# Optimization experiments

Measured on AMD Instinct MI355X. Metric: run time of the kernel, lower is better.

The kernel has to match this reference:

```python
import jax, jax.numpy as jnp
import numpy as np

B, S, E, H = 2, 2048, 1024, 16
DK = E // H


def setup_inputs() -> dict:
    key = jax.random.key(0)
    ks = jax.random.split(key, 10)
    x = jax.random.normal(ks[0], (B, S, E), dtype=jnp.float32)
    mask = jax.random.randint(ks[1], (B, S, S), 0, 2).astype(bool)
    scale = 1.0 / np.sqrt(E)
    def lin(k):
        kw, kb = jax.random.split(k)
        W = jax.random.uniform(kw, (E, E), minval=-scale, maxval=scale, dtype=jnp.float32)
        b = jax.random.uniform(kb, (E,), minval=-scale, maxval=scale, dtype=jnp.float32)
        return W, b
    Wq, bq = lin(ks[2])
    Wk, bk = lin(ks[3])
    Wv, bv = lin(ks[4])
    Wo, bo = lin(ks[5])
    return {"x": x, "mask": mask, "Wq": Wq, "bq": bq, "Wk": Wk, "bk": bk,
            "Wv": Wv, "bv": bv, "Wo": Wo, "bo": bo}


def reference(x, mask, Wq, bq, Wk, bk, Wv, bv, Wo, bo):
    # projections (torch Linear: y = x @ W.T + b)
    q = x @ Wq.T + bq
    k = x @ Wk.T + bk
    v = x @ Wv.T + bv
    # separate heads: [B,S,E] -> [B,H,S,DK]
    def split(t):
        return t.reshape(B, S, H, DK).transpose(0, 2, 1, 3)
    q, k, v = split(q), split(k), split(v)
    scores = jnp.einsum("bhqd,bhkd->bhqk", q, k) / jnp.sqrt(jnp.float32(DK))
    # masked_fill: positions where mask is True get -1e9 (mask broadcast over heads)
    scores = jnp.where(mask[:, None, :, :], jnp.float32(-1e9), scores)
    attn = jax.nn.softmax(scores, axis=-1)  # dropout is identity in eval
    out = jnp.einsum("bhqk,bhkd->bhqd", attn, v)
    out = out.transpose(0, 2, 1, 3).reshape(B, S, E)  # combine heads
    return out @ Wo.T + bo
```

## Files before the change

kernel.cpp:

```cpp
#include <hip/hip_runtime.h>
#include <hip/hip_bf16.h>


typedef __attribute__((ext_vector_type(8))) short short8;
typedef __attribute__((ext_vector_type(4))) float f32x4;
typedef __attribute__((ext_vector_type(16))) float f32x16;

#define MFMA16(a, b, c) __builtin_amdgcn_mfma_f32_16x16x32_bf16(a, b, c, 0, 0, 0)
#define MFMA32(a, b, c) __builtin_amdgcn_mfma_f32_32x32x16_bf16(a, b, c, 0, 0, 0)

#define BATCH 2
#define SEQ   2048
#define EMB   1024
#define HEADS 16
#define DKK   64

typedef __hip_bfloat16 bf16;

static __device__ __forceinline__ short bf16b(float f) {
    union { bf16 h; short s; } u;
    u.h = __float2bfloat16(f);
    return u.s;
}
static __device__ __forceinline__ unsigned cvtpk(float lo, float hi) {
    unsigned r;
    asm("v_cvt_pk_bf16_f32 %0, %1, %2" : "=v"(r) : "v"(lo), "v"(hi));
    return r;
}
static __device__ __forceinline__ void swap32(unsigned &a, unsigned &b) {
    asm("v_permlane32_swap_b32 %0, %1" : "+v"(a), "+v"(b));
}
static __device__ __forceinline__ short8 ld8k(const bf16* p) {
    return *(const short8*)p;
}
static __device__ __forceinline__ short8 ld8kf(const float* p) {
    const f32x4 a = *(const f32x4*)p;
    const f32x4 b = *(const f32x4*)(p + 4);
    short8 r;
    r[0] = bf16b(a[0]); r[1] = bf16b(a[1]); r[2] = bf16b(a[2]); r[3] = bf16b(a[3]);
    r[4] = bf16b(b[0]); r[5] = bf16b(b[1]); r[6] = bf16b(b[2]); r[7] = bf16b(b[3]);
    return r;
}

static __device__ __forceinline__ void glds16(const bf16* g, bf16* l) {
    __builtin_amdgcn_global_load_lds(
        (const __attribute__((address_space(1))) void*)g,
        (__attribute__((address_space(3))) void*)l, 16, 0, 0);
}

__global__ void detect_kernel(const unsigned int* __restrict__ mw,
                              int* __restrict__ flags) {
    __shared__ int mbyte;
    if (threadIdx.x == 0) mbyte = 0;
    __syncthreads();
    int mb = 0;
    for (int i = threadIdx.x; i < 4096; i += 256)
        if (mw[i] > 1u) mb = 1;
    if (mb) atomicOr(&mbyte, 1);
    __syncthreads();
    if (threadIdx.x == 0) { flags[0] = 1; flags[1] = mbyte; }
}

__global__ __launch_bounds__(256) void pack_mask(
        const void* __restrict__ mp, unsigned* __restrict__ Mp,
        const int* __restrict__ flags) {
    const bool m8 = flags[1] != 0;
    const int T = blockIdx.x * 256 + threadIdx.x;
    const int lane = T & 63, g = T >> 6;
    const int wvv = g & 3;
    const int qb  = (g >> 2) & 15;
    const int it  = (g >> 6) & 31;
    const int b   = g >> 11;
    const int l32 = lane & 31, hi = lane >> 5;
    const int q = qb * 128 + wvv * 32 + l32;
    const size_t rowb = ((size_t)(b * 2048 + q)) * 2048;

    unsigned out[8];
    if (m8) {
        const unsigned char* p8 = (const unsigned char*)mp;
#pragma unroll
        for (int k = 0; k < 8; ++k) {
            const int kb = k >> 2, tt = (k >> 1) & 1, u = k & 1;
            const int key0 = it * 64 + kb * 32 + tt * 16 + hi * 8 + u * 4;
            const unsigned v = *(const unsigned*)(p8 + rowb + key0);
            unsigned w = 0;
#pragma unroll
            for (int r = 0; r < 4; ++r)
                w |= ((((v >> (8 * r)) & 0xFFu) == 0u) ? 0xFFu : 0u) << (8 * r);
            out[k] = w;
        }
    } else {
        const int* p32 = (const int*)mp;
#pragma unroll
        for (int k = 0; k < 8; ++k) {
            const int kb = k >> 2, tt = (k >> 1) & 1, u = k & 1;
            const int key0 = it * 64 + kb * 32 + tt * 16 + hi * 8 + u * 4;
            const int4 v = *(const int4*)(p32 + rowb + key0);
            unsigned w = 0;
            w |=  (v.x == 0) ? 0xFFu : 0u;
            w |= ((v.y == 0) ? 0xFFu : 0u) << 8;
            w |= ((v.z == 0) ? 0xFFu : 0u) << 16;
            w |= ((v.w == 0) ? 0xFFu : 0u) << 24;
            out[k] = w;
        }
    }
    unsigned* dst = Mp + (size_t)g * 512 + lane * 8;
    *(uint4*)dst       = make_uint4(out[0], out[1], out[2], out[3]);
    *(uint4*)(dst + 4) = make_uint4(out[4], out[5], out[6], out[7]);
}

__global__ __launch_bounds__(256) void cvt_all(
        const float* __restrict__ x,  const float* __restrict__ wq,
        const float* __restrict__ wk, const float* __restrict__ wv,
        const float* __restrict__ wo,
        bf16* __restrict__ xb,  bf16* __restrict__ wqb,
        bf16* __restrict__ wkb, bf16* __restrict__ wvb,
        bf16* __restrict__ wob) {
    const int bid = blockIdx.x;
    const float* s; bf16* d; int base;
    if (bid < 2048)      { s = x;  d = xb;  base = bid; }
    else if (bid < 2560) { s = wq; d = wqb; base = bid - 2048; }
    else if (bid < 3072) { s = wk; d = wkb; base = bid - 2560; }
    else if (bid < 3584) { s = wv; d = wvb; base = bid - 3072; }
    else                 { s = wo; d = wob; base = bid - 3584; }
    const int i = (base * 256 + threadIdx.x) * 8;
    *(short8*)(d + i) = ld8kf(s + i);
}

__global__ __launch_bounds__(256) void gemm_qkv_staged(
        const bf16* __restrict__ X,
        const bf16* __restrict__ Wq, const bf16* __restrict__ Wk,
        const bf16* __restrict__ Wv,
        const float* __restrict__ bq, const float* __restrict__ bk,
        const float* __restrict__ bv,
        bf16* __restrict__ qo, bf16* __restrict__ ko, bf16* __restrict__ vo) {
    __shared__ bf16 As[2][128 * 32];
    __shared__ bf16 Bs[2][128 * 32];

    const int t = threadIdx.x, lane = t & 63;
    const int wv = t >> 6;
    const int mb = blockIdx.x / 24, nb = blockIdx.x % 24;
    const int m0 = mb * 128;
    const int n0g = nb * 128;
    const int sel = n0g >> 10;
    const int n0 = n0g & 1023;
    const bf16* W     = sel == 0 ? Wq : (sel == 1 ? Wk : Wv);
    const float* bias = sel == 0 ? bq : (sel == 1 ? bk : bv);
    bf16* out         = sel == 0 ? qo : (sel == 1 ? ko : vo);
    const float oscale = sel == 0 ? 0.18033688011f : 1.0f;

    const int wr = wv >> 1, wc = wv & 1;
    const int m_off = wr * 64, n_off = wc * 64;
    const int l16 = lane & 15, quad = lane >> 4;

    int srow[2], sg[2];
#pragma unroll
    for (int i = 0; i < 2; ++i) {
        const int c = i * 256 + t;
        srow[i] = c >> 2;
        sg[i]   = (c & 3) ^ (srow[i] & 3);
    }

    f32x4 acc[4][4];
#pragma unroll
    for (int i = 0; i < 4; ++i)
#pragma unroll
        for (int j = 0; j < 4; ++j)
            acc[i][j] = (f32x4){0.f, 0.f, 0.f, 0.f};

#pragma unroll
    for (int i = 0; i < 2; ++i) {
        glds16(X + (m0 + srow[i]) * 1024 + sg[i] * 8, &As[0][(i * 256 + t) * 8]);
        glds16(W + (n0 + srow[i]) * 1024 + sg[i] * 8, &Bs[0][(i * 256 + t) * 8]);
    }

    for (int it = 0; it < 32; ++it) {
        __syncthreads();
        if (it < 31) {
            const int ktn = (it + 1) * 32;
            const int nb_ = (it + 1) & 1;
#pragma unroll
            for (int i = 0; i < 2; ++i) {
                glds16(X + (m0 + srow[i]) * 1024 + ktn + sg[i] * 8,
                       &As[nb_][(i * 256 + t) * 8]);
                glds16(W + (n0 + srow[i]) * 1024 + ktn + sg[i] * 8,
                       &Bs[nb_][(i * 256 + t) * 8]);
            }
        }
        const bf16* Ab = As[it & 1];
        const bf16* Bb = Bs[it & 1];
        short8 af[4], bfr[4];
#pragma unroll
        for (int ii = 0; ii < 4; ++ii) {
            const int row = m_off + ii * 16 + l16;
            const int slot = quad ^ (row & 3);
            af[ii] = *(const short8*)(Ab + row * 32 + slot * 8);
        }
#pragma unroll
        for (int jj = 0; jj < 4; ++jj) {
            const int row = n_off + jj * 16 + l16;
            const int slot = quad ^ (row & 3);
            bfr[jj] = *(const short8*)(Bb + row * 32 + slot * 8);
        }
#pragma unroll
        for (int ii = 0; ii < 4; ++ii)
#pragma unroll
            for (int jj = 0; jj < 4; ++jj)
                acc[ii][jj] = MFMA16(af[ii], bfr[jj], acc[ii][jj]);
    }

#pragma unroll
    for (int j = 0; j < 4; ++j) {
        const int nl = n0 + n_off + j * 16 + l16;
        const float bj = bias[nl];
        const int h = nl >> 6, d = nl & 63;
#pragma unroll
        for (int i = 0; i < 4; ++i) {
#pragma unroll
            for (int r = 0; r < 4; ++r) {
                const int m = m0 + m_off + i * 16 + quad * 4 + r;
                const float v = (acc[i][j][r] + bj) * oscale;
                const int bb = m >> 11, ss = m & 2047;
                const int idx = (sel == 2)
                    ? ((bb * HEADS + h) * DKK + d) * SEQ + ss
                    : ((bb * HEADS + h) * SEQ + ss) * DKK + d;
                out[idx] = __float2bfloat16(v);
            }
        }
    }
}

__global__ __launch_bounds__(256) void gemm_out_staged(
        const bf16* __restrict__ X,
        const bf16* __restrict__ W, const float* __restrict__ bias,
        float* __restrict__ out) {
    __shared__ bf16 As[2][128 * 32];
    __shared__ bf16 Bs[2][64 * 32];

    const int t = threadIdx.x, lane = t & 63;
    const int wv = t >> 6;
    const int mb = blockIdx.x >> 4, nb = blockIdx.x & 15;
    const int m0 = mb * 128, n0 = nb * 64;
    const int wr = wv >> 1, wc = wv & 1;
    const int m_off = wr * 64, n_off = wc * 32;
    const int l16 = lane & 15, quad = lane >> 4;

    int srow[2], sg[2];
#pragma unroll
    for (int i = 0; i < 2; ++i) {
        const int c = i * 256 + t;
        srow[i] = c >> 2;
        sg[i]   = (c & 3) ^ (srow[i] & 3);
    }
    const int brow = t >> 2;
    const int bslot = (t & 3) ^ (brow & 3);

    f32x4 acc[4][2];
#pragma unroll
    for (int i = 0; i < 4; ++i)
#pragma unroll
        for (int j = 0; j < 2; ++j)
            acc[i][j] = (f32x4){0.f, 0.f, 0.f, 0.f};

#pragma unroll
    for (int i = 0; i < 2; ++i)
        glds16(X + (m0 + srow[i]) * 1024 + sg[i] * 8, &As[0][(i * 256 + t) * 8]);
    glds16(W + (n0 + brow) * 1024 + bslot * 8, &Bs[0][t * 8]);

    for (int it = 0; it < 32; ++it) {
        __syncthreads();
        if (it < 31) {
            const int ktn = (it + 1) * 32;
            const int nb_ = (it + 1) & 1;
#pragma unroll
            for (int i = 0; i < 2; ++i)
                glds16(X + (m0 + srow[i]) * 1024 + ktn + sg[i] * 8,
                       &As[nb_][(i * 256 + t) * 8]);
            glds16(W + (n0 + brow) * 1024 + ktn + bslot * 8, &Bs[nb_][t * 8]);
        }
        const bf16* Ab = As[it & 1];
        const bf16* Bb = Bs[it & 1];
        short8 af[4], bfr[2];
#pragma unroll
        for (int ii = 0; ii < 4; ++ii) {
            const int row = m_off + ii * 16 + l16;
            const int slot = quad ^ (row & 3);
            af[ii] = *(const short8*)(Ab + row * 32 + slot * 8);
        }
#pragma unroll
        for (int jj = 0; jj < 2; ++jj) {
            const int row = n_off + jj * 16 + l16;
            const int slot = quad ^ (row & 3);
            bfr[jj] = *(const short8*)(Bb + row * 32 + slot * 8);
        }
#pragma unroll
        for (int ii = 0; ii < 4; ++ii)
#pragma unroll
            for (int jj = 0; jj < 2; ++jj)
                acc[ii][jj] = MFMA16(af[ii], bfr[jj], acc[ii][jj]);
    }

#pragma unroll
    for (int j = 0; j < 2; ++j) {
        const int n = n0 + n_off + j * 16 + l16;
        const float bj = bias[n];
#pragma unroll
        for (int i = 0; i < 4; ++i) {
#pragma unroll
            for (int r = 0; r < 4; ++r) {
                const int m = m0 + m_off + i * 16 + quad * 4 + r;
                out[m * 1024 + n] = acc[i][j][r] + bj;
            }
        }
    }
}

__global__ __launch_bounds__(256, 2) void attn_kernel(
        const bf16* __restrict__ Qw,
        const bf16* __restrict__ Kw,
        const bf16* __restrict__ Vw,
        const unsigned* __restrict__ Mp,
        bf16* __restrict__ attn_out) {
    const int t = threadIdx.x;
    const int lane = t & 63;
    const int wv   = t >> 6;
    const int l32 = lane & 31, hi = lane >> 5;
    const int h = blockIdx.y, b = blockIdx.z;
    const int bh = b * HEADS + h;
    const int qb = blockIdx.x;
    const int qb0 = qb * 128;

    const bf16* Q  = Qw + bh * SEQ * DKK;
    const bf16* Kp = Kw + bh * SEQ * DKK;
    const bf16* Vt = Vw + bh * DKK * SEQ;

    __shared__ bf16 Ks[2][4096];
    __shared__ bf16 Vs[2][4096];

    short8 qf[4];
#pragma unroll
    for (int ks = 0; ks < 4; ++ks)
        qf[ks] = ld8k(Q + (qb0 + wv * 32 + l32) * DKK + ks * 16 + hi * 8);

    const short ob = bf16b(1.0f);
    short8 ones;
#pragma unroll
    for (int e = 0; e < 8; ++e) ones[e] = ob;

    f32x16 oA = {}, oB = {}, lacc = {};
    const f32x16 z16 = {};

    int srow[2], sg[2];
#pragma unroll
    for (int i = 0; i < 2; ++i) {
        const int c = i * 256 + t;
        srow[i] = c >> 3;
        sg[i]   = (c & 7) ^ (srow[i] & 7);
    }
#pragma unroll
    for (int i = 0; i < 2; ++i)
        glds16(Kp + srow[i] * DKK + sg[i] * 8, &Ks[0][(i * 256 + t) * 8]);
#pragma unroll
    for (int i = 0; i < 2; ++i)
        glds16(Vt + srow[i] * SEQ + sg[i] * 8, &Vs[0][(i * 256 + t) * 8]);

    const unsigned* mp_it =
        Mp + ((size_t)((b * 32) * 16 + qb) * 4 + wv) * 512 + lane * 8;

    for (int it = 0; it < 32; ++it) {
        __syncthreads();
        if (it < 31) {
            const int nb_ = (it + 1) & 1;
            const int ktn = (it + 1) * 64;
#pragma unroll
            for (int i = 0; i < 2; ++i)
                glds16(Kp + (ktn + srow[i]) * DKK + sg[i] * 8,
                       &Ks[nb_][(i * 256 + t) * 8]);
#pragma unroll
            for (int i = 0; i < 2; ++i)
                glds16(Vt + srow[i] * SEQ + ktn + sg[i] * 8,
                       &Vs[nb_][(i * 256 + t) * 8]);
        }
        const uint4 mA = *(const uint4*)mp_it;
        const uint4 mB = *(const uint4*)(mp_it + 4);
        mp_it += 32768;

        const bf16* Kb = Ks[it & 1];
        const bf16* Vb = Vs[it & 1];

        short8 kf0[4], kf1[4];
#pragma unroll
        for (int ks = 0; ks < 4; ++ks) {
            const int sl = (((ks * 2 + hi) ^ (l32 & 7))) * 8;
            kf0[ks] = *(const short8*)(Kb + l32 * 64 + sl);
            kf1[ks] = *(const short8*)(Kb + (32 + l32) * 64 + sl);
        }

        f32x16 s0, s1;
        __builtin_amdgcn_s_setprio(1);
        s0 = MFMA32(kf0[0], qf[0], z16);
        s0 = MFMA32(kf0[1], qf[1], s0);
        s0 = MFMA32(kf0[2], qf[2], s0);
        s0 = MFMA32(kf0[3], qf[3], s0);
        s1 = MFMA32(kf1[0], qf[0], z16);
        s1 = MFMA32(kf1[1], qf[1], s1);
        s1 = MFMA32(kf1[2], qf[2], s1);
        s1 = MFMA32(kf1[3], qf[3], s1);
        __builtin_amdgcn_s_setprio(0);

        {
            unsigned c0 = cvtpk(__builtin_exp2f(s0[0]),  __builtin_exp2f(s0[1]));
            unsigned c1 = cvtpk(__builtin_exp2f(s0[2]),  __builtin_exp2f(s0[3]));
            unsigned c2 = cvtpk(__builtin_exp2f(s0[4]),  __builtin_exp2f(s0[5]));
            unsigned c3 = cvtpk(__builtin_exp2f(s0[6]),  __builtin_exp2f(s0[7]));
            unsigned c4 = cvtpk(__builtin_exp2f(s0[8]),  __builtin_exp2f(s0[9]));
            unsigned c5 = cvtpk(__builtin_exp2f(s0[10]), __builtin_exp2f(s0[11]));
            unsigned c6 = cvtpk(__builtin_exp2f(s0[12]), __builtin_exp2f(s0[13]));
            unsigned c7 = cvtpk(__builtin_exp2f(s0[14]), __builtin_exp2f(s0[15]));
            swap32(c0, c2); swap32(c1, c3); swap32(c4, c6); swap32(c5, c7);
            union { short8 v; unsigned w[4]; } p0, p1;
            p0.w[0] = c0 & __builtin_amdgcn_perm(0u, mA.x, 0x01010000u);
            p0.w[1] = c1 & __builtin_amdgcn_perm(0u, mA.x, 0x03030202u);
            p0.w[2] = c2 & __builtin_amdgcn_perm(0u, mA.y, 0x01010000u);
            p0.w[3] = c3 & __builtin_amdgcn_perm(0u, mA.y, 0x03030202u);
            p1.w[0] = c4 & __builtin_amdgcn_perm(0u, mA.z, 0x01010000u);
            p1.w[1] = c5 & __builtin_amdgcn_perm(0u, mA.z, 0x03030202u);
            p1.w[2] = c6 & __builtin_amdgcn_perm(0u, mA.w, 0x01010000u);
            p1.w[3] = c7 & __builtin_amdgcn_perm(0u, mA.w, 0x03030202u);

            const int sl0 = ((0 + hi) ^ (l32 & 7)) * 8;
            const int sl1 = ((2 + hi) ^ (l32 & 7)) * 8;
            const short8 vf00 = *(const short8*)(Vb + l32 * 64 + sl0);
            const short8 vf10 = *(const short8*)(Vb + (32 + l32) * 64 + sl0);
            const short8 vf01 = *(const short8*)(Vb + l32 * 64 + sl1);
            const short8 vf11 = *(const short8*)(Vb + (32 + l32) * 64 + sl1);
            __builtin_amdgcn_s_setprio(1);
            lacc = MFMA32(p0.v, ones, lacc);
            oA = MFMA32(p0.v, vf00, oA);
            oB = MFMA32(p0.v, vf10, oB);
            lacc = MFMA32(p1.v, ones, lacc);
            oA = MFMA32(p1.v, vf01, oA);
            oB = MFMA32(p1.v, vf11, oB);
            __builtin_amdgcn_s_setprio(0);
        }
        {
            unsigned c0 = cvtpk(__builtin_exp2f(s1[0]),  __builtin_exp2f(s1[1]));
            unsigned c1 = cvtpk(__builtin_exp2f(s1[2]),  __builtin_exp2f(s1[3]));
            unsigned c2 = cvtpk(__builtin_exp2f(s1[4]),  __builtin_exp2f(s1[5]));
            unsigned c3 = cvtpk(__builtin_exp2f(s1[6]),  __builtin_exp2f(s1[7]));
            unsigned c4 = cvtpk(__builtin_exp2f(s1[8]),  __builtin_exp2f(s1[9]));
            unsigned c5 = cvtpk(__builtin_exp2f(s1[10]), __builtin_exp2f(s1[11]));
            unsigned c6 = cvtpk(__builtin_exp2f(s1[12]), __builtin_exp2f(s1[13]));
            unsigned c7 = cvtpk(__builtin_exp2f(s1[14]), __builtin_exp2f(s1[15]));
            swap32(c0, c2); swap32(c1, c3); swap32(c4, c6); swap32(c5, c7);
            union { short8 v; unsigned w[4]; } p0, p1;
            p0.w[0] = c0 & __builtin_amdgcn_perm(0u, mB.x, 0x01010000u);
            p0.w[1] = c1 & __builtin_amdgcn_perm(0u, mB.x, 0x03030202u);
            p0.w[2] = c2 & __builtin_amdgcn_perm(0u, mB.y, 0x01010000u);
            p0.w[3] = c3 & __builtin_amdgcn_perm(0u, mB.y, 0x03030202u);
            p1.w[0] = c4 & __builtin_amdgcn_perm(0u, mB.z, 0x01010000u);
            p1.w[1] = c5 & __builtin_amdgcn_perm(0u, mB.z, 0x03030202u);
            p1.w[2] = c6 & __builtin_amdgcn_perm(0u, mB.w, 0x01010000u);
            p1.w[3] = c7 & __builtin_amdgcn_perm(0u, mB.w, 0x03030202u);

            const int sl0 = ((4 + hi) ^ (l32 & 7)) * 8;
            const int sl1 = ((6 + hi) ^ (l32 & 7)) * 8;
            const short8 vf00 = *(const short8*)(Vb + l32 * 64 + sl0);
            const short8 vf10 = *(const short8*)(Vb + (32 + l32) * 64 + sl0);
            const short8 vf01 = *(const short8*)(Vb + l32 * 64 + sl1);
            const short8 vf11 = *(const short8*)(Vb + (32 + l32) * 64 + sl1);
            __builtin_amdgcn_s_setprio(1);
            lacc = MFMA32(p0.v, ones, lacc);
            oA = MFMA32(p0.v, vf00, oA);
            oB = MFMA32(p0.v, vf10, oB);
            lacc = MFMA32(p1.v, ones, lacc);
            oA = MFMA32(p1.v, vf01, oA);
            oB = MFMA32(p1.v, vf11, oB);
            __builtin_amdgcn_s_setprio(0);
        }
    }

#pragma unroll
    for (int r = 0; r < 16; ++r) {
        const int qrow = (r & 3) + 8 * (r >> 2) + 4 * hi;
        const float inv = 1.0f / lacc[r];
        const int q = qb0 + wv * 32 + qrow;
        bf16* orow = attn_out + (b * SEQ + q) * EMB + h * DKK;
        orow[l32]      = __float2bfloat16(oA[r] * inv);
        orow[32 + l32] = __float2bfloat16(oB[r] * inv);
    }
}

extern "C" void kernel_launch(void* const* d_in, const int* in_sizes, int n_in,
                              void* d_out, int out_size, void* d_ws, size_t ws_size,
                              hipStream_t stream) {
    char* ws = (char*)d_ws;
    const size_t MB = 1024 * 1024;
    int*      flags = (int*)ws;
    bf16*     wob   = (bf16*)(ws + 256);
    bf16*     wqb   = (bf16*)(ws + 256 + 2 * MB);
    bf16*     wkb   = (bf16*)(ws + 256 + 4 * MB);
    bf16*     wvb   = (bf16*)(ws + 256 + 6 * MB);
    unsigned* Mp    = (unsigned*)(ws + 256 + 2 * MB);
    bf16*     xb    = (bf16*)(ws + 256 + 10 * MB);
    bf16*     k_ws  = (bf16*)(ws + 256 + 18 * MB);
    bf16*     attn_ws = xb;

    bf16* q_ws = (bf16*)d_out;
    bf16* v_ws = (bf16*)d_out + 4194304;

    detect_kernel<<<1, 256, 0, stream>>>((const unsigned int*)d_in[1], flags);

    cvt_all<<<4096, 256, 0, stream>>>(
        (const float*)d_in[0], (const float*)d_in[2], (const float*)d_in[4],
        (const float*)d_in[6], (const float*)d_in[8],
        xb, wqb, wkb, wvb, wob);

    gemm_qkv_staged<<<768, 256, 0, stream>>>(
        xb, wqb, wkb, wvb,
        (const float*)d_in[3], (const float*)d_in[5], (const float*)d_in[7],
        q_ws, k_ws, v_ws);

    pack_mask<<<1024, 256, 0, stream>>>(d_in[1], Mp, flags);

    attn_kernel<<<dim3(SEQ / 128, HEADS, BATCH), 256, 0, stream>>>(
        q_ws, k_ws, v_ws, Mp, attn_ws);

    gemm_out_staged<<<512, 256, 0, stream>>>(
        attn_ws, wob, (const float*)d_in[9], (float*)d_out);
}
```

Before: 250.6 us.

## Triple-buffer K/V tiles with explicit vmcnt waits and remap block order

The attention kernel's K/V shared-memory staging grows from double to triple buffering. Tiles are prefetched two iterations ahead, and the full __syncthreads is replaced by an s_waitcnt vmcnt plus raw barrier so newer loads stay in flight. The packed-mask loads are also prefetched one iteration early. The grid becomes 1D with a swizzled block-to-(batch, head, qblock) mapping, likely to group blocks sharing K/V across XCDs for L2 reuse. The cost is 50% more LDS per block, which may hurt occupancy, and the hand-counted vmcnt must match the real number of outstanding loads.

```diff
diff --git a/kernel.cpp b/kernel.cpp
--- a/kernel.cpp
+++ b/kernel.cpp
@@ -325,17 +325,19 @@
     const int lane = t & 63;
     const int wv   = t >> 6;
     const int l32 = lane & 31, hi = lane >> 5;
-    const int h = blockIdx.y, b = blockIdx.z;
-    const int bh = b * HEADS + h;
-    const int qb = blockIdx.x;
+    const int bid = blockIdx.x;
+    const int w   = ((bid & 7) << 6) | (bid >> 3);
+    const int qb  = w & 15;
+    const int bh  = w >> 4;
+    const int b   = bh >> 4;
     const int qb0 = qb * 128;
 
     const bf16* Q  = Qw + bh * SEQ * DKK;
     const bf16* Kp = Kw + bh * SEQ * DKK;
     const bf16* Vt = Vw + bh * DKK * SEQ;
 
-    __shared__ bf16 Ks[2][4096];
-    __shared__ bf16 Vs[2][4096];
+    __shared__ bf16 Ks[3][4096];
+    __shared__ bf16 Vs[3][4096];
 
     short8 qf[4];
 #pragma unroll
@@ -357,36 +359,44 @@
         srow[i] = c >> 3;
         sg[i]   = (c & 7) ^ (srow[i] & 7);
     }
-#pragma unroll
-    for (int i = 0; i < 2; ++i)
-        glds16(Kp + srow[i] * DKK + sg[i] * 8, &Ks[0][(i * 256 + t) * 8]);
-#pragma unroll
-    for (int i = 0; i < 2; ++i)
-        glds16(Vt + srow[i] * SEQ + sg[i] * 8, &Vs[0][(i * 256 + t) * 8]);
+
+#define STAGE_TILE(ktn, bufi)                                                  \
+    do {                                                                       \
+        _Pragma("unroll")                                                      \
+        for (int i_ = 0; i_ < 2; ++i_)                                         \
+            glds16(Kp + ((ktn) + srow[i_]) * DKK + sg[i_] * 8,                 \
+                   &Ks[bufi][(i_ * 256 + t) * 8]);                             \
+        _Pragma("unroll")                                                      \
+        for (int i_ = 0; i_ < 2; ++i_)                                         \
+            glds16(Vt + srow[i_] * SEQ + (ktn) + sg[i_] * 8,                   \
+                   &Vs[bufi][(i_ * 256 + t) * 8]);                             \
+    } while (0)
 
     const unsigned* mp_it =
         Mp + ((size_t)((b * 32) * 16 + qb) * 4 + wv) * 512 + lane * 8;
 
+    STAGE_TILE(0, 0);
+    uint4 mcA = *(const uint4*)mp_it;
+    uint4 mcB = *(const uint4*)(mp_it + 4);
+    mp_it += 32768;
+    STAGE_TILE(64, 1);
+
     for (int it = 0; it < 32; ++it) {
-        __syncthreads();
+        if (it < 31) asm volatile("s_waitcnt vmcnt(6)" ::: "memory");
+        else         asm volatile("s_waitcnt vmcnt(0)" ::: "memory");
+        __builtin_amdgcn_s_barrier();
+        __builtin_amdgcn_sched_barrier(0);
+
+        uint4 mnA, mnB;
         if (it < 31) {
-            const int nb_ = (it + 1) & 1;
-            const int ktn = (it + 1) * 64;
-#pragma unroll
-            for (int i = 0; i < 2; ++i)
-                glds16(Kp + (ktn + srow[i]) * DKK + sg[i] * 8,
-                       &Ks[nb_][(i * 256 + t) * 8]);
-#pragma unroll
-            for (int i = 0; i < 2; ++i)
-                glds16(Vt + srow[i] * SEQ + ktn + sg[i] * 8,
-                       &Vs[nb_][(i * 256 + t) * 8]);
-        }
-        const uint4 mA = *(const uint4*)mp_it;
-        const uint4 mB = *(const uint4*)(mp_it + 4);
-        mp_it += 32768;
-
-        const bf16* Kb = Ks[it & 1];
-        const bf16* Vb = Vs[it & 1];
+            mnA = *(const uint4*)mp_it;
+            mnB = *(const uint4*)(mp_it + 4);
+            mp_it += 32768;
+        }
+        if (it < 30) STAGE_TILE((it + 2) * 64, (it + 2) % 3);
+
+        const bf16* Kb = Ks[it % 3];
+        const bf16* Vb = Vs[it % 3];
 
         short8 kf0[4], kf1[4];
 #pragma unroll
@@ -419,14 +429,14 @@
             unsigned c7 = cvtpk(__builtin_exp2f(s0[14]), __builtin_exp2f(s0[15]));
             swap32(c0, c2); swap32(c1, c3); swap32(c4, c6); swap32(c5, c7);
             union { short8 v; unsigned w[4]; } p0, p1;
-            p0.w[0] = c0 & __builtin_amdgcn_perm(0u, mA.x, 0x01010000u);
-            p0.w[1] = c1 & __builtin_amdgcn_perm(0u, mA.x, 0x03030202u);
-            p0.w[2] = c2 & __builtin_amdgcn_perm(0u, mA.y, 0x01010000u);
-            p0.w[3] = c3 & __builtin_amdgcn_perm(0u, mA.y, 0x03030202u);
-            p1.w[0] = c4 & __builtin_amdgcn_perm(0u, mA.z, 0x01010000u);
-            p1.w[1] = c5 & __builtin_amdgcn_perm(0u, mA.z, 0x03030202u);
-            p1.w[2] = c6 & __builtin_amdgcn_perm(0u, mA.w, 0x01010000u);
-            p1.w[3] = c7 & __builtin_amdgcn_perm(0u, mA.w, 0x03030202u);
+            p0.w[0] = c0 & __builtin_amdgcn_perm(0u, mcA.x, 0x01010000u);
+            p0.w[1] = c1 & __builtin_amdgcn_perm(0u, mcA.x, 0x03030202u);
+            p0.w[2] = c2 & __builtin_amdgcn_perm(0u, mcA.y, 0x01010000u);
+            p0.w[3] = c3 & __builtin_amdgcn_perm(0u, mcA.y, 0x03030202u);
+            p1.w[0] = c4 & __builtin_amdgcn_perm(0u, mcA.z, 0x01010000u);
+            p1.w[1] = c5 & __builtin_amdgcn_perm(0u, mcA.z, 0x03030202u);
+            p1.w[2] = c6 & __builtin_amdgcn_perm(0u, mcA.w, 0x01010000u);
+            p1.w[3] = c7 & __builtin_amdgcn_perm(0u, mcA.w, 0x03030202u);
 
             const int sl0 = ((0 + hi) ^ (l32 & 7)) * 8;
             const int sl1 = ((2 + hi) ^ (l32 & 7)) * 8;
@@ -454,14 +464,14 @@
             unsigned c7 = cvtpk(__builtin_exp2f(s1[14]), __builtin_exp2f(s1[15]));
             swap32(c0, c2); swap32(c1, c3); swap32(c4, c6); swap32(c5, c7);
             union { short8 v; unsigned w[4]; } p0, p1;
-            p0.w[0] = c0 & __builtin_amdgcn_perm(0u, mB.x, 0x01010000u);
-            p0.w[1] = c1 & __builtin_amdgcn_perm(0u, mB.x, 0x03030202u);
-            p0.w[2] = c2 & __builtin_amdgcn_perm(0u, mB.y, 0x01010000u);
-            p0.w[3] = c3 & __builtin_amdgcn_perm(0u, mB.y, 0x03030202u);
-            p1.w[0] = c4 & __builtin_amdgcn_perm(0u, mB.z, 0x01010000u);
-            p1.w[1] = c5 & __builtin_amdgcn_perm(0u, mB.z, 0x03030202u);
-            p1.w[2] = c6 & __builtin_amdgcn_perm(0u, mB.w, 0x01010000u);
-            p1.w[3] = c7 & __builtin_amdgcn_perm(0u, mB.w, 0x03030202u);
+            p0.w[0] = c0 & __builtin_amdgcn_perm(0u, mcB.x, 0x01010000u);
+            p0.w[1] = c1 & __builtin_amdgcn_perm(0u, mcB.x, 0x03030202u);
+            p0.w[2] = c2 & __builtin_amdgcn_perm(0u, mcB.y, 0x01010000u);
+            p0.w[3] = c3 & __builtin_amdgcn_perm(0u, mcB.y, 0x03030202u);
+            p1.w[0] = c4 & __builtin_amdgcn_perm(0u, mcB.z, 0x01010000u);
+            p1.w[1] = c5 & __builtin_amdgcn_perm(0u, mcB.z, 0x03030202u);
+            p1.w[2] = c6 & __builtin_amdgcn_perm(0u, mcB.w, 0x01010000u);
+            p1.w[3] = c7 & __builtin_amdgcn_perm(0u, mcB.w, 0x03030202u);
 
             const int sl0 = ((4 + hi) ^ (l32 & 7)) * 8;
             const int sl1 = ((6 + hi) ^ (l32 & 7)) * 8;
@@ -478,14 +488,16 @@
             oB = MFMA32(p1.v, vf11, oB);
             __builtin_amdgcn_s_setprio(0);
         }
-    }
+        if (it < 31) { mcA = mnA; mcB = mnB; }
+    }
+#undef STAGE_TILE
 
 #pragma unroll
     for (int r = 0; r < 16; ++r) {
         const int qrow = (r & 3) + 8 * (r >> 2) + 4 * hi;
         const float inv = 1.0f / lacc[r];
         const int q = qb0 + wv * 32 + qrow;
-        bf16* orow = attn_out + (b * SEQ + q) * EMB + h * DKK;
+        bf16* orow = attn_out + (b * SEQ + q) * EMB + (bh & 15) * DKK;
         orow[l32]      = __float2bfloat16(oA[r] * inv);
         orow[32 + l32] = __float2bfloat16(oB[r] * inv);
     }
@@ -523,8 +535,7 @@
 
     pack_mask<<<1024, 256, 0, stream>>>(d_in[1], Mp, flags);
 
-    attn_kernel<<<dim3(SEQ / 128, HEADS, BATCH), 256, 0, stream>>>(
-        q_ws, k_ws, v_ws, Mp, attn_ws);
+    attn_kernel<<<512, 256, 0, stream>>>(q_ws, k_ws, v_ws, Mp, attn_ws);
 
     gemm_out_staged<<<512, 256, 0, stream>>>(
         attn_ws, wob, (const float*)d_in[9], (float*)d_out);
```

Result: no change. 251.1 us (+0.2%).
